# Performance work log

Measured on AMD Instinct MI355X. Metric: run time of the kernel, lower is better.

The kernel has to match this reference:

```python
import jax, jax.numpy as jnp
import numpy as np

E = 8       # num experts
TOPK = 2    # top-k routing
R = 16      # lora rank
D = 2048    # d_model
F = 5632    # ffn hidden
B, S = 4, 2048


def setup_inputs() -> dict:
    key = jax.random.key(0)
    ks = jax.random.split(key, 11)
    sc = 0.02
    return {
        "x": jax.random.normal(ks[0], (B, S, D), jnp.float32),
        "gate_w": jax.random.normal(ks[1], (E, D), jnp.float32) * sc,
        "W1": jax.random.normal(ks[2], (F, D), jnp.float32) * sc,
        "W3": jax.random.normal(ks[3], (F, D), jnp.float32) * sc,
        "W2": jax.random.normal(ks[4], (D, F), jnp.float32) * sc,
        "A1": jax.random.normal(ks[5], (E, R, D), jnp.float32) * sc,
        "B1": jax.random.normal(ks[6], (E, F, R), jnp.float32) * sc,
        "A3": jax.random.normal(ks[7], (E, R, D), jnp.float32) * sc,
        "B3": jax.random.normal(ks[8], (E, F, R), jnp.float32) * sc,
        "A2": jax.random.normal(ks[9], (E, R, F), jnp.float32) * sc,
        "B2": jax.random.normal(ks[10], (E, D, R), jnp.float32) * sc,
    }


def reference(x, gate_w, W1, W3, W2, A1, B1, A3, B3, A2, B2):
    b, s, d = x.shape
    h = x.reshape(-1, d)                              # [T, D] tokens
    # --- BasicMoe routing (fp32 softmax, top-k, renormalize) ---
    router_logits = h @ gate_w.T                      # [T, E]
    probs = jax.nn.softmax(router_logits.astype(jnp.float32), axis=-1)
    w, sel = jax.lax.top_k(probs, TOPK)               # [T, K]
    w = w / jnp.sum(w, axis=-1, keepdims=True)
    w = w.astype(h.dtype)
    # per-token per-expert combine coefficient [T, E] (0 if not routed)
    coef = jnp.sum(jax.nn.one_hot(sel, E, dtype=w.dtype) * w[..., None], axis=1)
    # --- shared base projections (expert-independent) ---
    base1 = h @ W1.T                                  # [T, F]
    base3 = h @ W3.T                                  # [T, F]
    out = jnp.zeros_like(h)
    # small fixed loop over experts; dense-masked equivalent of gather/scatter
    for e in range(E):
        u1 = base1 + (h @ A1[e].T) @ B1[e].T          # w1 + loraB1(loraA1(x))
        u3 = base3 + (h @ A3[e].T) @ B3[e].T
        g = jax.nn.silu(u1) * u3                      # SwiGLU gate
        y = g @ W2.T + (g @ A2[e].T) @ B2[e].T        # w2 + lora2
        out = out + coef[:, e:e + 1] * y
    return out.reshape(b, s, d), router_logits
```

## Files before the change

kernel.cpp:

```cpp
#include <hip/hip_runtime.h>
#include <hip/hip_bf16.h>
#include <stdint.h>

#define TT   8192
#define DD   2048
#define FF   5632
#define EE   8
#define RR   16
#define NALL 11520
#define NPAIR 16384

typedef float  f32x4  __attribute__((ext_vector_type(4)));
typedef __bf16 bf16x8 __attribute__((ext_vector_type(8)));
typedef __bf16 bf16x4 __attribute__((ext_vector_type(4)));

#define AS1CAST(p) ((__attribute__((address_space(1))) void*)(p))
#define AS3CAST(p) ((__attribute__((address_space(3))) void*)(p))

__global__ __launch_bounds__(256) void cvt_f32_bf16(const float* __restrict__ src,
                                                    __bf16* __restrict__ dst, int n4) {
    int stride = gridDim.x * 256;
    for (int i = blockIdx.x * 256 + threadIdx.x; i < n4; i += stride) {
        float4 v = ((const float4*)src)[i];
        bf16x4 o = {(__bf16)v.x, (__bf16)v.y, (__bf16)v.z, (__bf16)v.w};
        ((bf16x4*)dst)[i] = o;
    }
}

__global__ __launch_bounds__(256) void cvt_A13(const float* __restrict__ A1,
                                               const float* __restrict__ A3,
                                               __bf16* __restrict__ dst) {
    int i = blockIdx.x * 256 + threadIdx.x;
    int col4 = i & 511;
    int j = i >> 9;
    int e = j >> 5, l = j & 31;
    const float* src = (l < 16) ? (A1 + (size_t)(e * 16 + l) * DD)
                                : (A3 + (size_t)(e * 16 + (l - 16)) * DD);
    float4 v = ((const float4*)src)[col4];
    bf16x4 o = {(__bf16)v.x, (__bf16)v.y, (__bf16)v.z, (__bf16)v.w};
    ((bf16x4*)(dst + (size_t)j * DD))[col4] = o;
}

__global__ __launch_bounds__(256) void cvt_A2t(const float* __restrict__ A2,
                                               __bf16* __restrict__ A2t) {
    int i = blockIdx.x * 256 + threadIdx.x;
    int f = i % FF;
    int r = (i / FF) % RR;
    int e = i / (FF * RR);
    A2t[((size_t)e * FF + f) * RR + r] = (__bf16)A2[i];
}

__global__ __launch_bounds__(256) void router_k(const float* __restrict__ x,
                                                const float* __restrict__ gw,
                                                float* __restrict__ logits,
                                                int* __restrict__ pair_e,
                                                float* __restrict__ pair_w) {
    int t = blockIdx.x * 4 + (threadIdx.x >> 6);
    int lane = threadIdx.x & 63;
    const float* xr = x + (size_t)t * DD;
    float acc[EE];
#pragma unroll
    for (int e = 0; e < EE; e++) acc[e] = 0.f;
    for (int d = lane; d < DD; d += 64) {
        float xv = xr[d];
#pragma unroll
        for (int e = 0; e < EE; e++) acc[e] += xv * gw[e * DD + d];
    }
#pragma unroll
    for (int off = 32; off > 0; off >>= 1) {
#pragma unroll
        for (int e = 0; e < EE; e++) acc[e] += __shfl_down(acc[e], off, 64);
    }
    if (lane == 0) {
        float mx = acc[0];
#pragma unroll
        for (int e = 1; e < EE; e++) mx = fmaxf(mx, acc[e]);
        float p[EE];
#pragma unroll
        for (int e = 0; e < EE; e++) p[e] = __expf(acc[e] - mx);
        int e0 = 0;
#pragma unroll
        for (int e = 1; e < EE; e++) if (p[e] > p[e0]) e0 = e;
        int e1 = (e0 == 0) ? 1 : 0;
#pragma unroll
        for (int e = 0; e < EE; e++) if (e != e0 && p[e] > p[e1]) e1 = e;
        float s = p[e0] + p[e1];
        pair_e[2 * t] = e0;     pair_e[2 * t + 1] = e1;
        pair_w[2 * t] = p[e0] / s; pair_w[2 * t + 1] = p[e1] / s;
#pragma unroll
        for (int e = 0; e < EE; e++) logits[(size_t)t * EE + e] = acc[e];
    }
}

template <int MODE>
__global__ __launch_bounds__(512, 2) void gemm256(const __bf16* __restrict__ A,
                                                  const __bf16* __restrict__ B,
                                                  void* __restrict__ Cv,
                                                  int M, int N, int K,
                                                  const float* __restrict__ GA,
                                                  const float* __restrict__ B2,
                                                  const int* __restrict__ pe,
                                                  int tbase) {
    __shared__ __align__(16) __bf16 lds[8][8192];
    char* const sbase = (char*)&lds[0][0];
    const int tid = threadIdx.x;
    const int w = tid >> 6, lane = tid & 63;
    const int lrow = lane & 15, lq = lane >> 4;
    const int wr = w >> 2, wc = w & 3;

    const int gx = gridDim.x;
    const int nwg = gx * gridDim.y;
    const int orig = blockIdx.x + blockIdx.y * gx;
    const int q8 = nwg >> 3, r8 = nwg & 7;
    const int xcd = orig & 7, sid = orig >> 3;
    const int nid = (xcd < r8 ? xcd * (q8 + 1) : r8 * (q8 + 1) + (xcd - r8) * q8) + sid;
    const int m0 = (nid % gx) * 256;
    const int n0 = (nid / gx) * 256;

    const size_t ldb = (size_t)K * 2;
    const int rq0 = w * 16 + (lane >> 3);
    const int cbs = ((lane & 7) * 16) ^ (((rq0 >> 2) & 1) << 5);
    const char* gA0 = (const char*)A + (size_t)(m0 + rq0) * ldb + cbs;
    const char* gA1 = gA0 + (size_t)128 * ldb;
    const char* gB0 = (const char*)B + (size_t)(n0 + rq0) * ldb + cbs;
    const char* gB1 = gB0 + (size_t)128 * ldb;
    const int wseg = w * 2048;

    const int sb = ((lrow >> 2) & 1) << 5;
    const int aoff = lrow * 128 + ((lq * 16) ^ sb);
    const int boff = ((wc & 1) * 64 + lrow) * 128 + ((lq * 16) ^ sb);
    const int abuf = wr;
    const int bbuf = 2 + (wc >> 1);

    f32x4 acc[8][4] = {};
    bf16x8 aR[4][2], aS[4][2], bR[2][2], bS[2][2];

#define GLDS(gp, lo) __builtin_amdgcn_global_load_lds(AS1CAST((void*)(gp)), AS3CAST(sbase + (lo)), 16, 0, 0)
#define STAGEM(gp, bufmh) do { const char* _g = (gp); \
        GLDS(_g, (bufmh) * 16384 + wseg); \
        GLDS(_g + 8 * ldb, (bufmh) * 16384 + wseg + 1024); } while (0)
#define LDAf(c, i, ks) (*(const bf16x8*)(sbase + ((c) * 4 + abuf) * 16384 + aoff + (i) * 2048 + (ks) * 64))
#define LDBf(c, j, ks) (*(const bf16x8*)(sbase + ((c) * 4 + bbuf) * 16384 + boff + (j) * 2048 + (ks) * 64))
#define MM(i, j, fa, fb) acc[i][j] = __builtin_amdgcn_mfma_f32_16x16x32_bf16(fa, fb, acc[i][j], 0, 0, 0)
#define PH_MID() do { __builtin_amdgcn_s_barrier(); \
        asm volatile("s_waitcnt lgkmcnt(0)" ::: "memory"); \
        __builtin_amdgcn_sched_barrier(0); \
        __builtin_amdgcn_s_setprio(1); } while (0)
#define PH_END() do { __builtin_amdgcn_s_setprio(0); \
        __builtin_amdgcn_s_barrier(); } while (0)

#define DO4(c, kBC, kAC) do { \
    _Pragma("unroll") for (int i = 0; i < 4; i++) { aR[i][0] = LDAf(c, i, 0); aR[i][1] = LDAf(c, i, 1); } \
    _Pragma("unroll") for (int j = 0; j < 2; j++) { bR[j][0] = LDBf(c, j, 0); bR[j][1] = LDBf(c, j, 1); } \
    STAGEM(gB0 + (size_t)(kBC) * 128, ((c) ^ 1) * 4 + 2); \
    PH_MID(); \
    _Pragma("unroll") for (int i = 0; i < 4; i++) \
    _Pragma("unroll") for (int j = 0; j < 2; j++) { MM(i, j, aR[i][0], bR[j][0]); MM(i, j, aR[i][1], bR[j][1]); } \
    PH_END(); \
    _Pragma("unroll") for (int i = 0; i < 4; i++) { aS[i][0] = LDAf(c, 4 + i, 0); aS[i][1] = LDAf(c, 4 + i, 1); } \
    STAGEM(gB1 + (size_t)(kBC) * 128, ((c) ^ 1) * 4 + 3); \
    PH_MID(); \
    _Pragma("unroll") for (int i = 0; i < 4; i++) \
    _Pragma("unroll") for (int j = 0; j < 2; j++) { MM(4 + i, j, aS[i][0], bR[j][0]); MM(4 + i, j, aS[i][1], bR[j][1]); } \
    PH_END(); \
    _Pragma("unroll") for (int j = 0; j < 2; j++) { bS[j][0] = LDBf(c, 2 + j, 0); bS[j][1] = LDBf(c, 2 + j, 1); } \
    STAGEM(gA0 + (size_t)(kAC) * 128, (c) * 4 + 0); \
    PH_MID(); \
    _Pragma("unroll") for (int i = 0; i < 4; i++) \
    _Pragma("unroll") for (int j = 0; j < 2; j++) { MM(i, 2 + j, aR[i][0], bS[j][0]); MM(i, 2 + j, aR[i][1], bS[j][1]); } \
    PH_END(); \
    STAGEM(gA1 + (size_t)(kAC) * 128, (c) * 4 + 1); \
    asm volatile("s_waitcnt vmcnt(4)" ::: "memory"); \
    PH_MID(); \
    _Pragma("unroll") for (int i = 0; i < 4; i++) \
    _Pragma("unroll") for (int j = 0; j < 2; j++) { MM(4 + i, 2 + j, aS[i][0], bS[j][0]); MM(4 + i, 2 + j, aS[i][1], bS[j][1]); } \
    PH_END(); \
} while (0)

    const int NT = K >> 6;
    const int NI = NT >> 1;

    STAGEM(gA0, 0); STAGEM(gA1, 1); STAGEM(gB0, 2); STAGEM(gB1, 3);
    STAGEM(gA0 + 128, 4); STAGEM(gA1 + 128, 5);
    asm volatile("s_waitcnt vmcnt(4)" ::: "memory");
    __builtin_amdgcn_s_barrier();

    for (int it = 0; it < NI; it++) {
        int k2 = 2 * it + 2; if (k2 > NT - 1) k2 = NT - 1;
        int k3 = 2 * it + 3; if (k3 > NT - 1) k3 = NT - 1;
        DO4(0, 2 * it + 1, k2);
        DO4(1, k2, k3);
    }

    asm volatile("s_waitcnt vmcnt(0)" ::: "memory");

#undef DO4
#undef PH_END
#undef PH_MID
#undef MM
#undef LDBf
#undef LDAf
#undef STAGEM
#undef GLDS

    if (MODE == 1) {
#pragma unroll
        for (int i = 0; i < 8; i++)
#pragma unroll
            for (int j = 0; j < 4; j++)
#pragma unroll
                for (int r = 0; r < 4; r++) {
                    int row = m0 + wr * 128 + i * 16 + lq * 4 + r;
                    int col = n0 + wc * 64 + j * 16 + lrow;
                    ((__bf16*)Cv)[(size_t)row * N + col] = (__bf16)acc[i][j][r];
                }
    } else {
#pragma unroll
        for (int i = 0; i < 8; i++) {
#pragma unroll
            for (int r = 0; r < 4; r++) {
                const int row = m0 + wr * 128 + i * 16 + lq * 4 + r;
                const int t = tbase + row;
                const int e0 = pe[2 * t], e1 = pe[2 * t + 1];
                const float4* g0p = (const float4*)(GA + (size_t)(2 * t) * RR);
                const float4* g1p = (const float4*)(GA + (size_t)(2 * t + 1) * RR);
                float4 ga0[4] = {g0p[0], g0p[1], g0p[2], g0p[3]};
                float4 ga1[4] = {g1p[0], g1p[1], g1p[2], g1p[3]};
                const float* B2e0 = B2 + (size_t)e0 * DD * RR;
                const float* B2e1 = B2 + (size_t)e1 * DD * RR;
#pragma unroll
                for (int j = 0; j < 4; j++) {
                    const int col = n0 + wc * 64 + j * 16 + lrow;
                    float l = acc[i][j][r];
                    const float4* b0 = (const float4*)(B2e0 + (size_t)col * RR);
                    const float4* b1 = (const float4*)(B2e1 + (size_t)col * RR);
#pragma unroll
                    for (int q = 0; q < 4; q++) {
                        float4 v0 = b0[q], v1 = b1[q];
                        l += ga0[q].x * v0.x + ga0[q].y * v0.y + ga0[q].z * v0.z + ga0[q].w * v0.w;
                        l += ga1[q].x * v1.x + ga1[q].y * v1.y + ga1[q].z * v1.z + ga1[q].w * v1.w;
                    }
                    ((float*)Cv)[(size_t)t * N + col] = l;
                }
            }
        }
    }
}

__global__ __launch_bounds__(256) void g_build_tok(const __bf16* __restrict__ base,
                                                   const __bf16* __restrict__ B1t,
                                                   const __bf16* __restrict__ B3t,
                                                   const __bf16* __restrict__ A2t,
                                                   const int* __restrict__ pair_e,
                                                   const float* __restrict__ pair_w,
                                                   __bf16* __restrict__ G,
                                                   float* __restrict__ GA,
                                                   int t0) {
    const int wave = threadIdx.x >> 6, lane = threadIdx.x & 63;
    const int lt = blockIdx.x * 4 + wave;
    const int t = t0 + lt;
    const int e0 = pair_e[2 * t], e1 = pair_e[2 * t + 1];
    const float w0 = pair_w[2 * t], w1 = pair_w[2 * t + 1];
    const __bf16* brow = base + (size_t)lt * NALL;

    float ha1a[16], ha3a[16], ha1b[16], ha3b[16];
    {
        const bf16x8* pa = (const bf16x8*)(brow + 2 * FF + e0 * 32);
        const bf16x8* pb = (const bf16x8*)(brow + 2 * FF + e1 * 32);
        bf16x8 a0 = pa[0], a1 = pa[1], a2v = pa[2], a3v = pa[3];
        bf16x8 b0 = pb[0], b1v = pb[1], b2v = pb[2], b3v = pb[3];
#pragma unroll
        for (int r = 0; r < 8; r++) {
            ha1a[r] = (float)a0[r];  ha1a[8 + r] = (float)a1[r];
            ha3a[r] = (float)a2v[r]; ha3a[8 + r] = (float)a3v[r];
            ha1b[r] = (float)b0[r];  ha1b[8 + r] = (float)b1v[r];
            ha3b[r] = (float)b2v[r]; ha3b[8 + r] = (float)b3v[r];
        }
    }
    const __bf16* B1a = B1t + (size_t)e0 * FF * RR;
    const __bf16* B3a = B3t + (size_t)e0 * FF * RR;
    const __bf16* A2a = A2t + (size_t)e0 * FF * RR;
    const __bf16* B1b = B1t + (size_t)e1 * FF * RR;
    const __bf16* B3b = B3t + (size_t)e1 * FF * RR;
    const __bf16* A2b = A2t + (size_t)e1 * FF * RR;
    __bf16* Grow = G + (size_t)lt * FF;

    float ga0[16], ga1[16];
#pragma unroll
    for (int r = 0; r < 16; r++) { ga0[r] = 0.f; ga1[r] = 0.f; }

    for (int f = lane; f < FF; f += 64) {
        const size_t fo = (size_t)f * RR;
        const bf16x8* p;
        p = (const bf16x8*)(B1a + fo); bf16x8 b1l = p[0], b1h = p[1];
        p = (const bf16x8*)(B3a + fo); bf16x8 b3l = p[0], b3h = p[1];
        p = (const bf16x8*)(B1b + fo); bf16x8 c1l = p[0], c1h = p[1];
        p = (const bf16x8*)(B3b + fo); bf16x8 c3l = p[0], c3h = p[1];
        float bb1 = (float)brow[f], bb3 = (float)brow[FF + f];
        float u1a = bb1, u3a = bb3, u1b = bb1, u3b = bb3;
#pragma unroll
        for (int r = 0; r < 8; r++) {
            u1a += ha1a[r] * (float)b1l[r] + ha1a[8 + r] * (float)b1h[r];
            u3a += ha3a[r] * (float)b3l[r] + ha3a[8 + r] * (float)b3h[r];
            u1b += ha1b[r] * (float)c1l[r] + ha1b[8 + r] * (float)c1h[r];
            u3b += ha3b[r] * (float)c3l[r] + ha3b[8 + r] * (float)c3h[r];
        }
        float g0 = (u1a / (1.f + __expf(-u1a))) * u3a;
        float g1 = (u1b / (1.f + __expf(-u1b))) * u3b;
        Grow[f] = (__bf16)(w0 * g0 + w1 * g1);
        p = (const bf16x8*)(A2a + fo); bf16x8 a2l = p[0], a2h = p[1];
        p = (const bf16x8*)(A2b + fo); bf16x8 a4l = p[0], a4h = p[1];
#pragma unroll
        for (int r = 0; r < 8; r++) {
            ga0[r]     += g0 * (float)a2l[r];
            ga0[8 + r] += g0 * (float)a2h[r];
            ga1[r]     += g1 * (float)a4l[r];
            ga1[8 + r] += g1 * (float)a4h[r];
        }
    }
#pragma unroll
    for (int off = 32; off > 0; off >>= 1) {
#pragma unroll
        for (int r = 0; r < 16; r++) {
            ga0[r] += __shfl_down(ga0[r], off, 64);
            ga1[r] += __shfl_down(ga1[r], off, 64);
        }
    }
    if (lane == 0) {
#pragma unroll
        for (int r = 0; r < 16; r++) {
            GA[(size_t)(2 * t) * RR + r]     = w0 * ga0[r];
            GA[(size_t)(2 * t + 1) * RR + r] = w1 * ga1[r];
        }
    }
}

extern "C" void kernel_launch(void* const* d_in, const int* in_sizes, int n_in,
                              void* d_out, int out_size, void* d_ws, size_t ws_size,
                              hipStream_t stream) {
    const float* x  = (const float*)d_in[0];
    const float* gw = (const float*)d_in[1];
    const float* W1 = (const float*)d_in[2];
    const float* W3 = (const float*)d_in[3];
    const float* W2 = (const float*)d_in[4];
    const float* A1 = (const float*)d_in[5];
    const float* B1 = (const float*)d_in[6];
    const float* A3 = (const float*)d_in[7];
    const float* B3 = (const float*)d_in[8];
    const float* A2 = (const float*)d_in[9];
    const float* B2 = (const float*)d_in[10];

    float* out    = (float*)d_out;
    float* logits = out + (size_t)TT * DD;

    char* ws = (char*)d_ws;
    size_t off = 0;
    auto carve = [&](size_t bytes) {
        char* p = ws + off;
        off += (bytes + 255) & ~(size_t)255;
        return p;
    };
    auto pad = [](size_t b) { return (b + 255) & ~(size_t)255; };

    __bf16* B1b   = (__bf16*)carve((size_t)EE * FF * RR * 2);
    __bf16* B3b   = (__bf16*)carve((size_t)EE * FF * RR * 2);
    __bf16* A2t   = (__bf16*)carve((size_t)EE * FF * RR * 2);
    float*  GA    = (float*)carve((size_t)NPAIR * RR * 4);
    int*    pair_e = (int*)carve((size_t)NPAIR * 4);
    float*  pair_w = (float*)carve((size_t)NPAIR * 4);
    char*   WREG  = carve((size_t)NALL * DD * 2);
    __bf16* W_all = (__bf16*)WREG;
    size_t base0 = off;

    int C = 0, full = 0;
    {
        const int cand[5] = {4096, 2048, 1024, 512, 256};
        for (int ci = 0; ci < 5; ci++) {
            int c = cand[ci];
            size_t need = base0 + pad((size_t)TT * FF * 2)
                        + pad((size_t)c * DD * 2) + pad((size_t)c * NALL * 2);
            if (need <= ws_size) { full = 1; C = c; break; }
        }
    }
    __bf16* Gbuf = nullptr; __bf16* base_c; __bf16* h_c; __bf16* W2b; __bf16* G_c = nullptr;
    if (full) {
        Gbuf   = (__bf16*)carve((size_t)TT * FF * 2);
        h_c    = (__bf16*)carve((size_t)C * DD * 2);
        base_c = (__bf16*)carve((size_t)C * NALL * 2);
        W2b    = (__bf16*)WREG;
    } else {
        W2b = (__bf16*)carve((size_t)DD * FF * 2);
        C = 2048;
        while (C > 256) {
            size_t need = off + pad((size_t)C * DD * 2)
                        + pad((size_t)C * NALL * 2) + pad((size_t)C * FF * 2);
            if (need <= ws_size) break;
            C >>= 1;
        }
        h_c    = (__bf16*)carve((size_t)C * DD * 2);
        base_c = (__bf16*)carve((size_t)C * NALL * 2);
        G_c    = (__bf16*)carve((size_t)C * FF * 2);
    }

    cvt_f32_bf16<<<1024, 256, 0, stream>>>(W1, W_all, FF * DD / 4);
    cvt_f32_bf16<<<1024, 256, 0, stream>>>(W3, W_all + (size_t)FF * DD, FF * DD / 4);
    cvt_A13<<<512, 256, 0, stream>>>(A1, A3, W_all + (size_t)2 * FF * DD);
    cvt_f32_bf16<<<512, 256, 0, stream>>>(B1, B1b, EE * FF * RR / 4);
    cvt_f32_bf16<<<512, 256, 0, stream>>>(B3, B3b, EE * FF * RR / 4);
    cvt_A2t<<<EE * RR * FF / 256, 256, 0, stream>>>(A2, A2t);
    if (!full) cvt_f32_bf16<<<1024, 256, 0, stream>>>(W2, W2b, DD * FF / 4);

    router_k<<<TT / 4, 256, 0, stream>>>(x, gw, logits, pair_e, pair_w);

    for (int t0 = 0; t0 < TT; t0 += C) {
        cvt_f32_bf16<<<1024, 256, 0, stream>>>(x + (size_t)t0 * DD, h_c, C * DD / 4);
        gemm256<1><<<dim3(C / 256, NALL / 256), 512, 0, stream>>>(
            h_c, W_all, base_c, C, NALL, DD, nullptr, nullptr, nullptr, 0);
        __bf16* Gp = full ? (Gbuf + (size_t)t0 * FF) : G_c;
        g_build_tok<<<C / 4, 256, 0, stream>>>(base_c, B1b, B3b, A2t, pair_e, pair_w, Gp, GA, t0);
        if (!full) {
            gemm256<2><<<dim3(C / 256, DD / 256), 512, 0, stream>>>(
                G_c, W2b, out, C, DD, FF, GA, B2, pair_e, t0);
        }
    }

    if (full) {
        cvt_f32_bf16<<<1024, 256, 0, stream>>>(W2, W2b, DD * FF / 4);
        gemm256<2><<<dim3(TT / 256, DD / 256), 512, 0, stream>>>(
            Gbuf, W2b, out, TT, DD, FF, GA, B2, pair_e, 0);
    }
}
```

Before: 1.353 ms.

## Fold LoRA-B2 projection into down GEMM by extending K with routed coefficients

The routed, weighted rank-16 LoRA activations are written as a 128-column bf16 tail on each G row, zero for non-selected experts. W2 is extended with the transposed B2 blocks, so a single GEMM with K=5760 computes both the base W2 product and the LoRA-B2 term. This replaces the scalar fp32 epilogue, which gathered B2 rows per output element, with a plain store. In exchange it adds about 2% more MACs, an extra conversion pass over B2, and bf16 rounding of the LoRA coefficients.

```diff
diff --git a/kernel.cpp b/kernel.cpp
--- a/kernel.cpp
+++ b/kernel.cpp
@@ -8,6 +8,7 @@
 #define EE   8
 #define RR   16
 #define NALL 11520
+#define KE   5760
 #define NPAIR 16384
 
 typedef float  f32x4  __attribute__((ext_vector_type(4)));
@@ -50,6 +51,28 @@
     A2t[((size_t)e * FF + f) * RR + r] = (__bf16)A2[i];
 }
 
+__global__ __launch_bounds__(256) void cvt_W2ext(const float* __restrict__ W2,
+                                                 const float* __restrict__ B2,
+                                                 __bf16* __restrict__ dst) {
+    const int n4 = DD * KE / 4;
+    int stride = gridDim.x * 256;
+    for (int i = blockIdx.x * 256 + threadIdx.x; i < n4; i += stride) {
+        int j = (i % (KE / 4)) * 4;
+        int d = i / (KE / 4);
+        float4 v;
+        if (j < FF) {
+            v = *(const float4*)(W2 + (size_t)d * FF + j);
+        } else {
+            int o = j - FF;
+            int e = o >> 4, r = o & 15;
+            const float* b = B2 + ((size_t)e * DD + d) * RR + r;
+            v.x = b[0]; v.y = b[1]; v.z = b[2]; v.w = b[3];
+        }
+        bf16x4 o4 = {(__bf16)v.x, (__bf16)v.y, (__bf16)v.z, (__bf16)v.w};
+        ((bf16x4*)dst)[i] = o4;
+    }
+}
+
 __global__ __launch_bounds__(256) void router_k(const float* __restrict__ x,
                                                 const float* __restrict__ gw,
                                                 float* __restrict__ logits,
@@ -92,15 +115,11 @@
     }
 }
 
-template <int MODE>
+template <int OUT_BF16>
 __global__ __launch_bounds__(512, 2) void gemm256(const __bf16* __restrict__ A,
                                                   const __bf16* __restrict__ B,
                                                   void* __restrict__ Cv,
-                                                  int M, int N, int K,
-                                                  const float* __restrict__ GA,
-                                                  const float* __restrict__ B2,
-                                                  const int* __restrict__ pe,
-                                                  int tbase) {
+                                                  int M, int N, int K) {
     __shared__ __align__(16) __bf16 lds[8][8192];
     char* const sbase = (char*)&lds[0][0];
     const int tid = threadIdx.x;
@@ -203,48 +222,18 @@
 #undef STAGEM
 #undef GLDS
 
-    if (MODE == 1) {
-#pragma unroll
-        for (int i = 0; i < 8; i++)
-#pragma unroll
-            for (int j = 0; j < 4; j++)
-#pragma unroll
-                for (int r = 0; r < 4; r++) {
-                    int row = m0 + wr * 128 + i * 16 + lq * 4 + r;
-                    int col = n0 + wc * 64 + j * 16 + lrow;
-                    ((__bf16*)Cv)[(size_t)row * N + col] = (__bf16)acc[i][j][r];
-                }
-    } else {
-#pragma unroll
-        for (int i = 0; i < 8; i++) {
+#pragma unroll
+    for (int i = 0; i < 8; i++)
+#pragma unroll
+        for (int j = 0; j < 4; j++)
 #pragma unroll
             for (int r = 0; r < 4; r++) {
-                const int row = m0 + wr * 128 + i * 16 + lq * 4 + r;
-                const int t = tbase + row;
-                const int e0 = pe[2 * t], e1 = pe[2 * t + 1];
-                const float4* g0p = (const float4*)(GA + (size_t)(2 * t) * RR);
-                const float4* g1p = (const float4*)(GA + (size_t)(2 * t + 1) * RR);
-                float4 ga0[4] = {g0p[0], g0p[1], g0p[2], g0p[3]};
-                float4 ga1[4] = {g1p[0], g1p[1], g1p[2], g1p[3]};
-                const float* B2e0 = B2 + (size_t)e0 * DD * RR;
-                const float* B2e1 = B2 + (size_t)e1 * DD * RR;
-#pragma unroll
-                for (int j = 0; j < 4; j++) {
-                    const int col = n0 + wc * 64 + j * 16 + lrow;
-                    float l = acc[i][j][r];
-                    const float4* b0 = (const float4*)(B2e0 + (size_t)col * RR);
-                    const float4* b1 = (const float4*)(B2e1 + (size_t)col * RR);
-#pragma unroll
-                    for (int q = 0; q < 4; q++) {
-                        float4 v0 = b0[q], v1 = b1[q];
-                        l += ga0[q].x * v0.x + ga0[q].y * v0.y + ga0[q].z * v0.z + ga0[q].w * v0.w;
-                        l += ga1[q].x * v1.x + ga1[q].y * v1.y + ga1[q].z * v1.z + ga1[q].w * v1.w;
-                    }
-                    ((float*)Cv)[(size_t)t * N + col] = l;
-                }
+                int row = m0 + wr * 128 + i * 16 + lq * 4 + r;
+                int col = n0 + wc * 64 + j * 16 + lrow;
+                float v = acc[i][j][r];
+                if (OUT_BF16) ((__bf16*)Cv)[(size_t)row * N + col] = (__bf16)v;
+                else          ((float*)Cv)[(size_t)row * N + col] = v;
             }
-        }
-    }
 }
 
 __global__ __launch_bounds__(256) void g_build_tok(const __bf16* __restrict__ base,
@@ -254,7 +243,6 @@
                                                    const int* __restrict__ pair_e,
                                                    const float* __restrict__ pair_w,
                                                    __bf16* __restrict__ G,
-                                                   float* __restrict__ GA,
                                                    int t0) {
     const int wave = threadIdx.x >> 6, lane = threadIdx.x & 63;
     const int lt = blockIdx.x * 4 + wave;
@@ -283,7 +271,7 @@
     const __bf16* B1b = B1t + (size_t)e1 * FF * RR;
     const __bf16* B3b = B3t + (size_t)e1 * FF * RR;
     const __bf16* A2b = A2t + (size_t)e1 * FF * RR;
-    __bf16* Grow = G + (size_t)lt * FF;
+    __bf16* Grow = G + (size_t)lt * KE;
 
     float ga0[16], ga1[16];
 #pragma unroll
@@ -327,10 +315,23 @@
         }
     }
     if (lane == 0) {
-#pragma unroll
-        for (int r = 0; r < 16; r++) {
-            GA[(size_t)(2 * t) * RR + r]     = w0 * ga0[r];
-            GA[(size_t)(2 * t + 1) * RR + r] = w1 * ga1[r];
+        __bf16* tail = Grow + FF;
+        bf16x8 z = {};
+#pragma unroll
+        for (int e = 0; e < EE; e++) {
+            if (e == e0) {
+                bf16x8 lo, hi;
+#pragma unroll
+                for (int r = 0; r < 8; r++) { lo[r] = (__bf16)(w0 * ga0[r]); hi[r] = (__bf16)(w0 * ga0[8 + r]); }
+                ((bf16x8*)(tail + e * 16))[0] = lo; ((bf16x8*)(tail + e * 16))[1] = hi;
+            } else if (e == e1) {
+                bf16x8 lo, hi;
+#pragma unroll
+                for (int r = 0; r < 8; r++) { lo[r] = (__bf16)(w1 * ga1[r]); hi[r] = (__bf16)(w1 * ga1[8 + r]); }
+                ((bf16x8*)(tail + e * 16))[0] = lo; ((bf16x8*)(tail + e * 16))[1] = hi;
+            } else {
+                ((bf16x8*)(tail + e * 16))[0] = z; ((bf16x8*)(tail + e * 16))[1] = z;
+            }
         }
     }
 }
@@ -365,7 +366,6 @@
     __bf16* B1b   = (__bf16*)carve((size_t)EE * FF * RR * 2);
     __bf16* B3b   = (__bf16*)carve((size_t)EE * FF * RR * 2);
     __bf16* A2t   = (__bf16*)carve((size_t)EE * FF * RR * 2);
-    float*  GA    = (float*)carve((size_t)NPAIR * RR * 4);
     int*    pair_e = (int*)carve((size_t)NPAIR * 4);
     float*  pair_w = (float*)carve((size_t)NPAIR * 4);
     char*   WREG  = carve((size_t)NALL * DD * 2);
@@ -377,29 +377,29 @@
         const int cand[5] = {4096, 2048, 1024, 512, 256};
         for (int ci = 0; ci < 5; ci++) {
             int c = cand[ci];
-            size_t need = base0 + pad((size_t)TT * FF * 2)
+            size_t need = base0 + pad((size_t)TT * KE * 2)
                         + pad((size_t)c * DD * 2) + pad((size_t)c * NALL * 2);
             if (need <= ws_size) { full = 1; C = c; break; }
         }
     }
-    __bf16* Gbuf = nullptr; __bf16* base_c; __bf16* h_c; __bf16* W2b; __bf16* G_c = nullptr;
+    __bf16* Gbuf = nullptr; __bf16* base_c; __bf16* h_c; __bf16* W2e; __bf16* G_c = nullptr;
     if (full) {
-        Gbuf   = (__bf16*)carve((size_t)TT * FF * 2);
+        Gbuf   = (__bf16*)carve((size_t)TT * KE * 2);
         h_c    = (__bf16*)carve((size_t)C * DD * 2);
         base_c = (__bf16*)carve((size_t)C * NALL * 2);
-        W2b    = (__bf16*)WREG;
+        W2e    = (__bf16*)WREG;
     } else {
-        W2b = (__bf16*)carve((size_t)DD * FF * 2);
+        W2e = (__bf16*)carve((size_t)DD * KE * 2);
         C = 2048;
         while (C > 256) {
             size_t need = off + pad((size_t)C * DD * 2)
-                        + pad((size_t)C * NALL * 2) + pad((size_t)C * FF * 2);
+                        + pad((size_t)C * NALL * 2) + pad((size_t)C * KE * 2);
             if (need <= ws_size) break;
             C >>= 1;
         }
         h_c    = (__bf16*)carve((size_t)C * DD * 2);
         base_c = (__bf16*)carve((size_t)C * NALL * 2);
-        G_c    = (__bf16*)carve((size_t)C * FF * 2);
+        G_c    = (__bf16*)carve((size_t)C * KE * 2);
     }
 
     cvt_f32_bf16<<<1024, 256, 0, stream>>>(W1, W_all, FF * DD / 4);
@@ -408,25 +408,25 @@
     cvt_f32_bf16<<<512, 256, 0, stream>>>(B1, B1b, EE * FF * RR / 4);
     cvt_f32_bf16<<<512, 256, 0, stream>>>(B3, B3b, EE * FF * RR / 4);
     cvt_A2t<<<EE * RR * FF / 256, 256, 0, stream>>>(A2, A2t);
-    if (!full) cvt_f32_bf16<<<1024, 256, 0, stream>>>(W2, W2b, DD * FF / 4);
+    if (!full) cvt_W2ext<<<2048, 256, 0, stream>>>(W2, B2, W2e);
 
     router_k<<<TT / 4, 256, 0, stream>>>(x, gw, logits, pair_e, pair_w);
 
     for (int t0 = 0; t0 < TT; t0 += C) {
         cvt_f32_bf16<<<1024, 256, 0, stream>>>(x + (size_t)t0 * DD, h_c, C * DD / 4);
         gemm256<1><<<dim3(C / 256, NALL / 256), 512, 0, stream>>>(
-            h_c, W_all, base_c, C, NALL, DD, nullptr, nullptr, nullptr, 0);
-        __bf16* Gp = full ? (Gbuf + (size_t)t0 * FF) : G_c;
-        g_build_tok<<<C / 4, 256, 0, stream>>>(base_c, B1b, B3b, A2t, pair_e, pair_w, Gp, GA, t0);
+            h_c, W_all, base_c, C, NALL, DD);
+        __bf16* Gp = full ? (Gbuf + (size_t)t0 * KE) : G_c;
+        g_build_tok<<<C / 4, 256, 0, stream>>>(base_c, B1b, B3b, A2t, pair_e, pair_w, Gp, t0);
         if (!full) {
-            gemm256<2><<<dim3(C / 256, DD / 256), 512, 0, stream>>>(
-                G_c, W2b, out, C, DD, FF, GA, B2, pair_e, t0);
+            gemm256<0><<<dim3(C / 256, DD / 256), 512, 0, stream>>>(
+                G_c, W2e, out + (size_t)t0 * DD, C, DD, KE);
         }
     }
 
     if (full) {
-        cvt_f32_bf16<<<1024, 256, 0, stream>>>(W2, W2b, DD * FF / 4);
-        gemm256<2><<<dim3(TT / 256, DD / 256), 512, 0, stream>>>(
-            Gbuf, W2b, out, TT, DD, FF, GA, B2, pair_e, 0);
-    }
-}
+        cvt_W2ext<<<2048, 256, 0, stream>>>(W2, B2, W2e);
+        gemm256<0><<<dim3(TT / 256, DD / 256), 512, 0, stream>>>(
+            Gbuf, W2e, out, TT, DD, KE);
+    }
+}
```

After: 1.243 ms. 8.2% less time.
